# Optimization experiments

Measured on AMD Instinct MI355X. Metric: run time of the kernel, lower is better.

Reference implementation:

```python
import jax, jax.numpy as jnp
import numpy as np

EPS = 1e-5

def setup_inputs() -> dict:
    key = jax.random.key(0)
    ks = jax.random.split(key, 8)
    N, D = 65536, 256
    x = jax.random.normal(ks[0], (N, D), dtype=jnp.float32)
    # BatchNorm1d affine params (frozen, torch default init)
    bn_gamma = jnp.ones((D,), jnp.float32)
    bn_beta = jnp.zeros((D,), jnp.float32)
    # Linear layers, torch default uniform(-1/sqrt(fan_in), 1/sqrt(fan_in))
    def lin(k, fin, fout):
        k1, k2 = jax.random.split(k)
        bound = 1.0 / np.sqrt(fin)
        W = jax.random.uniform(k1, (fout, fin), jnp.float32, -bound, bound)
        b = jax.random.uniform(k2, (fout,), jnp.float32, -bound, bound)
        return W, b
    W1, b1 = lin(ks[1], D, 512)
    W2, b2 = lin(ks[2], 512, 2048)
    Wf, bf = lin(ks[3], 2048, D)
    return {"x": x, "bn_gamma": bn_gamma, "bn_beta": bn_beta,
            "W1": W1, "b1": b1, "W2": W2, "b2": b2, "Wf": Wf, "bf": bf}


def reference(x, bn_gamma, bn_beta, W1, b1, W2, b2, Wf, bf):
    # BatchNorm1d in training mode: per-batch mean / biased variance
    mu = jnp.mean(x, axis=0)
    var = jnp.mean(jnp.square(x - mu), axis=0)
    xn = (x - mu) * jax.lax.rsqrt(var + EPS) * bn_gamma + bn_beta
    raw_feats = jnp.tanh(xn)
    h = xn @ W1.T + b1          # [N, 512]
    h = h @ W2.T + b2           # [N, 2048]
    out = jnp.tanh(h @ Wf.T + bf)  # [N, latent_dim]
    return (out, raw_feats)
```

## Files before the change

### kernel.cpp

```cpp
#include <hip/hip_runtime.h>
#include <hip/hip_bf16.h>
#include <stdint.h>

#define NROWS 65536
#define DFEAT 256

typedef __bf16 bf16x8 __attribute__((ext_vector_type(8)));
typedef float f32x4 __attribute__((ext_vector_type(4)));

__device__ __forceinline__ float fast_tanh(float x) {
    return 1.0f - 2.0f / (__expf(2.0f * x) + 1.0f);
}

__global__ void k1_kernel(const float4* __restrict__ x4,
                          float* __restrict__ sums,
                          float* __restrict__ sumsq,
                          const float* __restrict__ Wf,
                          const float* __restrict__ W2,
                          const float* __restrict__ b1,
                          const float* __restrict__ b2,
                          float* __restrict__ P,
                          float* __restrict__ u) {
    __shared__ float smem[2176];
    int t = threadIdx.x;
    int b = blockIdx.x;
    if (b < 512) {
        float (*ps)[256] = (float (*)[256])smem;
        float (*pq)[256] = (float (*)[256])(smem + 1024);
        int c4 = t & 63;
        int r  = t >> 6;
        size_t i0 = (size_t)b * 128;
        float4 s = make_float4(0.f, 0.f, 0.f, 0.f);
        float4 q = make_float4(0.f, 0.f, 0.f, 0.f);
        for (int i = r; i < 128; i += 4) {
            float4 v = x4[(i0 + i) * 64 + c4];
            s.x += v.x; s.y += v.y; s.z += v.z; s.w += v.w;
            q.x += v.x * v.x; q.y += v.y * v.y; q.z += v.z * v.z; q.w += v.w * v.w;
        }
        ps[r][c4 * 4 + 0] = s.x; ps[r][c4 * 4 + 1] = s.y;
        ps[r][c4 * 4 + 2] = s.z; ps[r][c4 * 4 + 3] = s.w;
        pq[r][c4 * 4 + 0] = q.x; pq[r][c4 * 4 + 1] = q.y;
        pq[r][c4 * 4 + 2] = q.z; pq[r][c4 * 4 + 3] = q.w;
        __syncthreads();
        float ts = ps[0][t] + ps[1][t] + ps[2][t] + ps[3][t];
        float tq = pq[0][t] + pq[1][t] + pq[2][t] + pq[3][t];
        atomicAdd(&sums[t], ts);
        atomicAdd(&sumsq[t], tq);
    } else if (b < 1024) {
        int bb = b - 512;
        int bj = (bb & 15) * 32;
        int bi = ((bb >> 4) & 7) * 32;
        int kb = (bb >> 7) * 512;
        float (*As)[33] = (float (*)[33])smem;
        float (*Bs)[33] = (float (*)[33])(smem + 1056);
        int tx = t & 15, ty = t >> 4;
        int row = t >> 3;
        int col = (t & 7) * 4;
        float acc00 = 0.f, acc01 = 0.f, acc10 = 0.f, acc11 = 0.f;
        for (int k0 = kb; k0 < kb + 512; k0 += 32) {
            float4 av = *(const float4*)&Wf[(size_t)(bi + row) * 2048 + k0 + col];
            As[row][col + 0] = av.x; As[row][col + 1] = av.y;
            As[row][col + 2] = av.z; As[row][col + 3] = av.w;
            float4 bv = *(const float4*)&W2[(size_t)(k0 + row) * 512 + bj + col];
            Bs[row][col + 0] = bv.x; Bs[row][col + 1] = bv.y;
            Bs[row][col + 2] = bv.z; Bs[row][col + 3] = bv.w;
            __syncthreads();
            #pragma unroll
            for (int k = 0; k < 32; ++k) {
                float a0 = As[ty * 2 + 0][k];
                float a1 = As[ty * 2 + 1][k];
                float b0 = Bs[k][tx * 2 + 0];
                float b1v = Bs[k][tx * 2 + 1];
                acc00 += a0 * b0; acc01 += a0 * b1v;
                acc10 += a1 * b0; acc11 += a1 * b1v;
            }
            __syncthreads();
        }
        int i = bi + ty * 2, j = bj + tx * 2;
        atomicAdd(&P[(size_t)(i + 0) * 512 + j + 0], acc00);
        atomicAdd(&P[(size_t)(i + 0) * 512 + j + 1], acc01);
        atomicAdd(&P[(size_t)(i + 1) * 512 + j + 0], acc10);
        atomicAdd(&P[(size_t)(i + 1) * 512 + j + 1], acc11);
    } else {
        int lane = t & 63;
        int row = (b - 1024) * 4 + (t >> 6);
        const float* Wr = W2 + (size_t)row * 512;
        float s = 0.f;
        for (int k = lane; k < 512; k += 64) s += Wr[k] * b1[k];
        #pragma unroll
        for (int off = 32; off; off >>= 1) s += __shfl_xor(s, off);
        if (lane == 0) u[row] = s + b2[row];
    }
}

__global__ void k2_kernel(const float* __restrict__ sums,
                          const float* __restrict__ sumsq,
                          const float* __restrict__ gamma,
                          const float* __restrict__ beta,
                          float* __restrict__ scl,
                          float* __restrict__ sft,
                          const float* __restrict__ P,
                          const float* __restrict__ W1,
                          const float* __restrict__ Wf,
                          const float* __restrict__ u,
                          const float* __restrict__ bfv,
                          __bf16* __restrict__ Bprep,
                          float* __restrict__ cv) {
    __shared__ float smem[2176];
    int t = threadIdx.x;
    int b = blockIdx.x;
    if (b >= 128) {
        const float invN = 1.0f / (float)NROWS;
        float mu  = sums[t] * invN;
        float var = sumsq[t] * invN - mu * mu;
        float rs  = rsqrtf(var + 1e-5f);
        float a   = gamma[t] * rs;
        scl[t] = a;
        sft[t] = beta[t] - mu * a;
        return;
    }
    if (b >= 64) {
        int lane = t & 63;
        int row = (b - 64) * 4 + (t >> 6);
        const float* Wr = Wf + (size_t)row * 2048;
        float s = 0.f;
        for (int k = lane; k < 2048; k += 64) s += Wr[k] * u[k];
        #pragma unroll
        for (int off = 32; off; off >>= 1) s += __shfl_xor(s, off);
        if (lane == 0) cv[row] = s + bfv[row];
        return;
    }
    float (*As)[33] = (float (*)[33])smem;
    float (*Bs)[33] = (float (*)[33])(smem + 1056);
    int tx = t & 15, ty = t >> 4;
    int bi = (b >> 3) * 32;
    int bj = (b & 7) * 32;
    int row = t >> 3;
    int col = (t & 7) * 4;
    float acc00 = 0.f, acc01 = 0.f, acc10 = 0.f, acc11 = 0.f;
    for (int k0 = 0; k0 < 512; k0 += 32) {
        float4 av = *(const float4*)&P[(size_t)(bi + row) * 512 + k0 + col];
        As[row][col + 0] = av.x; As[row][col + 1] = av.y;
        As[row][col + 2] = av.z; As[row][col + 3] = av.w;
        float4 bv = *(const float4*)&W1[(size_t)(k0 + row) * 256 + bj + col];
        Bs[row][col + 0] = bv.x; Bs[row][col + 1] = bv.y;
        Bs[row][col + 2] = bv.z; Bs[row][col + 3] = bv.w;
        __syncthreads();
        #pragma unroll
        for (int k = 0; k < 32; ++k) {
            float a0 = As[ty * 2 + 0][k];
            float a1 = As[ty * 2 + 1][k];
            float b0 = Bs[k][tx * 2 + 0];
            float b1v = Bs[k][tx * 2 + 1];
            acc00 += a0 * b0; acc01 += a0 * b1v;
            acc10 += a1 * b0; acc11 += a1 * b1v;
        }
        __syncthreads();
    }
    int j = bi + ty * 2, k = bj + tx * 2;
    float vals[2][2] = {{acc00, acc01}, {acc10, acc11}};
    #pragma unroll
    for (int dj = 0; dj < 2; ++dj)
        #pragma unroll
        for (int dk = 0; dk < 2; ++dk) {
            float v = vals[dj][dk];
            int jj = j + dj, kk = k + dk;
            __bf16 h = (__bf16)v;
            __bf16 lo = (__bf16)(v - (float)h);
            int kstep = kk >> 5, kgrp = (kk >> 3) & 3, e = kk & 7;
            Bprep[((((size_t)kstep * 2 + 0) * 4 + kgrp) * 256 + jj) * 8 + e] = h;
            Bprep[((((size_t)kstep * 2 + 1) * 4 + kgrp) * 256 + jj) * 8 + e] = lo;
        }
}

__global__ __launch_bounds__(256, 4)
void main_mfma(const float4* __restrict__ x4,
               const float* __restrict__ scl,
               const float* __restrict__ sft,
               const __bf16* __restrict__ Bprep,
               const float* __restrict__ cvec,
               float* __restrict__ out,
               float4* __restrict__ rf4) {
    __shared__ __align__(16) __bf16 Abuf[2][2][64][4][8];
    __shared__ float ss[256], sh[256];
    int t = threadIdx.x;
    int l = t & 63;
    int w = t >> 6;
    int g = l >> 4, li = l & 15;
    size_t row0 = (size_t)blockIdx.x * 64;
    int arow = t >> 2;
    int akg  = t & 3;

    ss[t] = scl[t];
    sh[t] = sft[t];

    f32x4 acc[4][4];
    #pragma unroll
    for (int i = 0; i < 4; ++i)
        #pragma unroll
        for (int j = 0; j < 4; ++j)
            acc[i][j] = (f32x4){0.f, 0.f, 0.f, 0.f};

    size_t xb = (row0 + arow) * 64 + akg * 2;
    float4 v0 = x4[xb];
    float4 v1 = x4[xb + 1];

    __syncthreads();

    #pragma unroll 2
    for (int s = 0; s < 8; ++s) {
        int kb = s * 32 + akg * 8;
        float4 sc0 = *(const float4*)&ss[kb], sc1 = *(const float4*)&ss[kb + 4];
        float4 sf0 = *(const float4*)&sh[kb], sf1 = *(const float4*)&sh[kb + 4];
        float xn[8];
        xn[0] = v0.x * sc0.x + sf0.x;
        xn[1] = v0.y * sc0.y + sf0.y;
        xn[2] = v0.z * sc0.z + sf0.z;
        xn[3] = v0.w * sc0.w + sf0.w;
        xn[4] = v1.x * sc1.x + sf1.x;
        xn[5] = v1.y * sc1.y + sf1.y;
        xn[6] = v1.z * sc1.z + sf1.z;
        xn[7] = v1.w * sc1.w + sf1.w;
        float4 r0, r1;
        r0.x = fast_tanh(xn[0]); r0.y = fast_tanh(xn[1]);
        r0.z = fast_tanh(xn[2]); r0.w = fast_tanh(xn[3]);
        r1.x = fast_tanh(xn[4]); r1.y = fast_tanh(xn[5]);
        r1.z = fast_tanh(xn[6]); r1.w = fast_tanh(xn[7]);
        rf4[xb + s * 8] = r0;
        rf4[xb + s * 8 + 1] = r1;
        bf16x8 hv, lv;
        #pragma unroll
        for (int e = 0; e < 8; ++e) {
            __bf16 h = (__bf16)xn[e];
            hv[e] = h;
            lv[e] = (__bf16)(xn[e] - (float)h);
        }
        *(bf16x8*)&Abuf[s & 1][0][arow][akg][0] = hv;
        *(bf16x8*)&Abuf[s & 1][1][arow][akg][0] = lv;
        if (s < 7) {
            v0 = x4[xb + (s + 1) * 8];
            v1 = x4[xb + (s + 1) * 8 + 1];
        }
        __syncthreads();

        bf16x8 ah[4], al[4];
        #pragma unroll
        for (int i = 0; i < 4; ++i) {
            ah[i] = *(const bf16x8*)&Abuf[s & 1][0][i * 16 + li][g][0];
            al[i] = *(const bf16x8*)&Abuf[s & 1][1][i * 16 + li][g][0];
        }
        const __bf16* bh_base = Bprep + (size_t)(8 * s + g) * 2048;
        const __bf16* bl_base = Bprep + (size_t)(8 * s + 4 + g) * 2048;
        #pragma unroll
        for (int j = 0; j < 4; ++j) {
            int coll = w * 64 + j * 16 + li;
            bf16x8 bh = *(const bf16x8*)&bh_base[(size_t)coll * 8];
            bf16x8 bl = *(const bf16x8*)&bl_base[(size_t)coll * 8];
            #pragma unroll
            for (int i = 0; i < 4; ++i) {
                acc[i][j] = __builtin_amdgcn_mfma_f32_16x16x32_bf16(ah[i], bh, acc[i][j], 0, 0, 0);
                acc[i][j] = __builtin_amdgcn_mfma_f32_16x16x32_bf16(al[i], bh, acc[i][j], 0, 0, 0);
                acc[i][j] = __builtin_amdgcn_mfma_f32_16x16x32_bf16(ah[i], bl, acc[i][j], 0, 0, 0);
            }
        }
    }

    #pragma unroll
    for (int j = 0; j < 4; ++j) {
        int gcol = w * 64 + j * 16 + li;
        float cj = cvec[gcol];
        #pragma unroll
        for (int i = 0; i < 4; ++i) {
            #pragma unroll
            for (int r = 0; r < 4; ++r) {
                size_t grow = row0 + i * 16 + g * 4 + r;
                out[grow * 256 + gcol] = fast_tanh(acc[i][j][r] + cj);
            }
        }
    }
}

extern "C" void kernel_launch(void* const* d_in, const int* in_sizes, int n_in,
                              void* d_out, int out_size, void* d_ws, size_t ws_size,
                              hipStream_t stream) {
    const float* x     = (const float*)d_in[0];
    const float* gamma = (const float*)d_in[1];
    const float* beta  = (const float*)d_in[2];
    const float* W1    = (const float*)d_in[3];
    const float* b1    = (const float*)d_in[4];
    const float* W2    = (const float*)d_in[5];
    const float* b2    = (const float*)d_in[6];
    const float* Wf    = (const float*)d_in[7];
    const float* bf    = (const float*)d_in[8];

    float* out = (float*)d_out;
    float* rf  = out + (size_t)NROWS * DFEAT;

    float* ws    = (float*)d_ws;
    float* sums  = ws;
    float* sumsq = ws + 256;
    float* P     = ws + 512;
    float* u     = ws + 131584;
    float* cv    = ws + 133632;
    float* scl   = ws + 133888;
    float* sft   = ws + 134144;
    __bf16* Bprep = (__bf16*)(ws + 134400);

    hipMemsetAsync(ws, 0, (size_t)131584 * sizeof(float), stream);

    k1_kernel<<<1536, 256, 0, stream>>>((const float4*)x, sums, sumsq,
                                        Wf, W2, b1, b2, P, u);
    k2_kernel<<<129, 256, 0, stream>>>(sums, sumsq, gamma, beta, scl, sft,
                                       P, W1, Wf, u, bf, Bprep, cv);
    main_mfma<<<NROWS / 64, 256, 0, stream>>>((const float4*)x, scl, sft,
                                              Bprep, cv, out, (float4*)rf);
}
```

Baseline: 264.6 us.

## Load A fragments directly from global per wave, drop LDS staging and barriers

Removes the shared-memory A tile and per-step __syncthreads. Each wave now loads and normalizes all 64 rows of x straight into MFMA register fragments, and only one wave per row group writes the tanh raw features. The intent is to cut the LDS round-trip and block-wide synchronisation. In exchange each x element is loaded and normalized four times, once per wave, and register pressure rises, so launch bounds are relaxed from 4 blocks per CU.

```diff
diff --git a/kernel.cpp b/kernel.cpp
--- a/kernel.cpp
+++ b/kernel.cpp
@@ -173,7 +173,7 @@
         }
 }
 
-__global__ __launch_bounds__(256, 4)
+__global__ __launch_bounds__(256)
 void main_mfma(const float4* __restrict__ x4,
                const float* __restrict__ scl,
                const float* __restrict__ sft,
@@ -181,15 +181,12 @@
                const float* __restrict__ cvec,
                float* __restrict__ out,
                float4* __restrict__ rf4) {
-    __shared__ __align__(16) __bf16 Abuf[2][2][64][4][8];
     __shared__ float ss[256], sh[256];
     int t = threadIdx.x;
     int l = t & 63;
     int w = t >> 6;
     int g = l >> 4, li = l & 15;
     size_t row0 = (size_t)blockIdx.x * 64;
-    int arow = t >> 2;
-    int akg  = t & 3;
 
     ss[t] = scl[t];
     sh[t] = sft[t];
@@ -201,66 +198,64 @@
         for (int j = 0; j < 4; ++j)
             acc[i][j] = (f32x4){0.f, 0.f, 0.f, 0.f};
 
-    size_t xb = (row0 + arow) * 64 + akg * 2;
-    float4 v0 = x4[xb];
-    float4 v1 = x4[xb + 1];
-
     __syncthreads();
 
-    #pragma unroll 2
     for (int s = 0; s < 8; ++s) {
-        int kb = s * 32 + akg * 8;
+        float4 xv[4][2];
+        #pragma unroll
+        for (int i = 0; i < 4; ++i) {
+            size_t base = (row0 + i * 16 + li) * 64 + s * 8 + g * 2;
+            xv[i][0] = x4[base];
+            xv[i][1] = x4[base + 1];
+        }
+        const __bf16* bh_base = Bprep + (size_t)(8 * s + g) * 2048;
+        const __bf16* bl_base = Bprep + (size_t)(8 * s + 4 + g) * 2048;
+        bf16x8 bh[4], bl[4];
+        #pragma unroll
+        for (int j = 0; j < 4; ++j) {
+            int coll = w * 64 + j * 16 + li;
+            bh[j] = *(const bf16x8*)&bh_base[(size_t)coll * 8];
+            bl[j] = *(const bf16x8*)&bl_base[(size_t)coll * 8];
+        }
+        int kb = s * 32 + g * 8;
         float4 sc0 = *(const float4*)&ss[kb], sc1 = *(const float4*)&ss[kb + 4];
         float4 sf0 = *(const float4*)&sh[kb], sf1 = *(const float4*)&sh[kb + 4];
-        float xn[8];
-        xn[0] = v0.x * sc0.x + sf0.x;
-        xn[1] = v0.y * sc0.y + sf0.y;
-        xn[2] = v0.z * sc0.z + sf0.z;
-        xn[3] = v0.w * sc0.w + sf0.w;
-        xn[4] = v1.x * sc1.x + sf1.x;
-        xn[5] = v1.y * sc1.y + sf1.y;
-        xn[6] = v1.z * sc1.z + sf1.z;
-        xn[7] = v1.w * sc1.w + sf1.w;
-        float4 r0, r1;
-        r0.x = fast_tanh(xn[0]); r0.y = fast_tanh(xn[1]);
-        r0.z = fast_tanh(xn[2]); r0.w = fast_tanh(xn[3]);
-        r1.x = fast_tanh(xn[4]); r1.y = fast_tanh(xn[5]);
-        r1.z = fast_tanh(xn[6]); r1.w = fast_tanh(xn[7]);
-        rf4[xb + s * 8] = r0;
-        rf4[xb + s * 8 + 1] = r1;
-        bf16x8 hv, lv;
-        #pragma unroll
-        for (int e = 0; e < 8; ++e) {
-            __bf16 h = (__bf16)xn[e];
-            hv[e] = h;
-            lv[e] = (__bf16)(xn[e] - (float)h);
-        }
-        *(bf16x8*)&Abuf[s & 1][0][arow][akg][0] = hv;
-        *(bf16x8*)&Abuf[s & 1][1][arow][akg][0] = lv;
-        if (s < 7) {
-            v0 = x4[xb + (s + 1) * 8];
-            v1 = x4[xb + (s + 1) * 8 + 1];
-        }
-        __syncthreads();
-
         bf16x8 ah[4], al[4];
         #pragma unroll
         for (int i = 0; i < 4; ++i) {
-            ah[i] = *(const bf16x8*)&Abuf[s & 1][0][i * 16 + li][g][0];
-            al[i] = *(const bf16x8*)&Abuf[s & 1][1][i * 16 + li][g][0];
-        }
-        const __bf16* bh_base = Bprep + (size_t)(8 * s + g) * 2048;
-        const __bf16* bl_base = Bprep + (size_t)(8 * s + 4 + g) * 2048;
+            float xn[8];
+            xn[0] = xv[i][0].x * sc0.x + sf0.x;
+            xn[1] = xv[i][0].y * sc0.y + sf0.y;
+            xn[2] = xv[i][0].z * sc0.z + sf0.z;
+            xn[3] = xv[i][0].w * sc0.w + sf0.w;
+            xn[4] = xv[i][1].x * sc1.x + sf1.x;
+            xn[5] = xv[i][1].y * sc1.y + sf1.y;
+            xn[6] = xv[i][1].z * sc1.z + sf1.z;
+            xn[7] = xv[i][1].w * sc1.w + sf1.w;
+            #pragma unroll
+            for (int e = 0; e < 8; ++e) {
+                __bf16 h = (__bf16)xn[e];
+                ah[i][e] = h;
+                al[i][e] = (__bf16)(xn[e] - (float)h);
+            }
+            if (i == w) {
+                float4 r0, r1;
+                r0.x = fast_tanh(xn[0]); r0.y = fast_tanh(xn[1]);
+                r0.z = fast_tanh(xn[2]); r0.w = fast_tanh(xn[3]);
+                r1.x = fast_tanh(xn[4]); r1.y = fast_tanh(xn[5]);
+                r1.z = fast_tanh(xn[6]); r1.w = fast_tanh(xn[7]);
+                size_t rbase = (row0 + w * 16 + li) * 64 + s * 8 + g * 2;
+                rf4[rbase] = r0;
+                rf4[rbase + 1] = r1;
+            }
+        }
         #pragma unroll
         for (int j = 0; j < 4; ++j) {
-            int coll = w * 64 + j * 16 + li;
-            bf16x8 bh = *(const bf16x8*)&bh_base[(size_t)coll * 8];
-            bf16x8 bl = *(const bf16x8*)&bl_base[(size_t)coll * 8];
             #pragma unroll
             for (int i = 0; i < 4; ++i) {
-                acc[i][j] = __builtin_amdgcn_mfma_f32_16x16x32_bf16(ah[i], bh, acc[i][j], 0, 0, 0);
-                acc[i][j] = __builtin_amdgcn_mfma_f32_16x16x32_bf16(al[i], bh, acc[i][j], 0, 0, 0);
-                acc[i][j] = __builtin_amdgcn_mfma_f32_16x16x32_bf16(ah[i], bl, acc[i][j], 0, 0, 0);
+                acc[i][j] = __builtin_amdgcn_mfma_f32_16x16x32_bf16(ah[i], bh[j], acc[i][j], 0, 0, 0);
+                acc[i][j] = __builtin_amdgcn_mfma_f32_16x16x32_bf16(al[i], bh[j], acc[i][j], 0, 0, 0);
+                acc[i][j] = __builtin_amdgcn_mfma_f32_16x16x32_bf16(ah[i], bl[j], acc[i][j], 0, 0, 0);
             }
         }
     }
```

Result: slower. 270.1 us (+2.1%).
